# Optimization experiments

Measured on AMD Instinct MI355X. Metric: run time of the kernel, lower is better.

The kernel has to match this reference:

```python
import jax, jax.numpy as jnp
import numpy as np


def conv1d(x, w, b):
    # x: (N, Cin, W), w: (Cout, Cin, K) -> (N, Cout, W-K+1), VALID conv (torch Conv1d)
    y = jax.lax.conv_general_dilated(x, w, (1,), 'VALID', dimension_numbers=('NCH', 'OIH', 'NCH'))
    return y + b[None, :, None]


def cnn_block(x, w, b):
    # conv1d then MaxPool1d over the full valid length -> (N, Cout)
    return jnp.max(conv1d(x, w, b), axis=2)


def highway(x, Wp, bp, Wg, bg):
    p = jax.nn.relu(x @ Wp.T + bp)
    g = jax.nn.sigmoid(x @ Wg.T + bg)
    return g * p + (1.0 - g) * x


def lstm_masked(x, lens, Wih, Whh, bih, bhh):
    # x: (N, Wt, E); lens: (N,) valid lengths. Emulates pack_padded_sequence +
    # nn.LSTM + pad_packed_sequence: outputs are h_t for t < len, zeros after.
    N, Wt, _ = x.shape
    H = Whh.shape[1]
    bias = bih + bhh
    h0 = jnp.zeros((N, H), x.dtype)

    def step(carry, inp):
        xt, t = inp
        h, c = carry
        z = xt @ Wih.T + h @ Whh.T + bias  # (N, 4H), gate order i,f,g,o
        i, f, g, o = jnp.split(z, 4, axis=-1)
        c2 = jax.nn.sigmoid(f) * c + jax.nn.sigmoid(i) * jnp.tanh(g)
        h2 = jax.nn.sigmoid(o) * jnp.tanh(c2)
        valid = (t < lens)[:, None]
        h2 = jnp.where(valid, h2, h)
        c2 = jnp.where(valid, c2, c)
        return (h2, c2), jnp.where(valid, h2, jnp.zeros_like(h2))

    xs = jnp.moveaxis(x, 1, 0)  # (Wt, N, E)
    ts = jnp.arange(Wt)
    _, out = jax.lax.scan(step, (h0, h0), (xs, ts))
    return jnp.moveaxis(out, 0, 1)  # (N, Wt, H)


def setup_inputs() -> dict:
    key = jax.random.key(0)
    ks = jax.random.split(key, 32)
    B, T = 32, 48
    WL, WA, WE = 33, 50, 30
    EL, EA, EE, H = 300, 988, 20, 128
    CL, CA, CE = 128, 256, 64
    s = 0.02
    inp = {
        'x_lin': jax.random.normal(ks[0], (B, T, WL, EL), jnp.float32),
        'x_aco': jax.random.normal(ks[1], (B, T, WA, EA), jnp.float32),
        'x_emo': jax.random.normal(ks[2], (B, T, WE, EE), jnp.float32),
        'window_length': jax.random.randint(ks[3], (B, T), 0, WE).astype(jnp.int32) + 1,
        'length': jax.random.randint(ks[4], (B,), 1, T + 1).astype(jnp.int32),
        # CNN params
        'convL_w': s * jax.random.normal(ks[5], (CL, EL, 5), jnp.float32),
        'convL_b': jnp.zeros((CL,), jnp.float32),
        'convA_w': s * jax.random.normal(ks[6], (CA, EA, 10), jnp.float32),
        'convA_b': jnp.zeros((CA,), jnp.float32),
        'convE_w': s * jax.random.normal(ks[7], (CE, H, 3), jnp.float32),
        'convE_b': jnp.zeros((CE,), jnp.float32),
        # Highway params
        'hwL_Wp': s * jax.random.normal(ks[8], (CL, CL), jnp.float32),
        'hwL_bp': jnp.zeros((CL,), jnp.float32),
        'hwL_Wg': s * jax.random.normal(ks[9], (CL, CL), jnp.float32),
        'hwL_bg': jnp.zeros((CL,), jnp.float32),
        'hwA_Wp': s * jax.random.normal(ks[10], (CA, CA), jnp.float32),
        'hwA_bp': jnp.zeros((CA,), jnp.float32),
        'hwA_Wg': s * jax.random.normal(ks[11], (CA, CA), jnp.float32),
        'hwA_bg': jnp.zeros((CA,), jnp.float32),
        'hwE_Wp': s * jax.random.normal(ks[12], (CE, CE), jnp.float32),
        'hwE_bp': jnp.zeros((CE,), jnp.float32),
        'hwE_Wg': s * jax.random.normal(ks[13], (CE, CE), jnp.float32),
        'hwE_bg': jnp.zeros((CE,), jnp.float32),
        # LSTM params (nn.LSTM, 1 layer, batch_first)
        'lstm_Wih': s * jax.random.normal(ks[14], (4 * H, EE), jnp.float32),
        'lstm_Whh': s * jax.random.normal(ks[15], (4 * H, H), jnp.float32),
        'lstm_bih': jnp.zeros((4 * H,), jnp.float32),
        'lstm_bhh': jnp.zeros((4 * H,), jnp.float32),
    }
    return inp


def reference(x_lin, x_aco, x_emo, window_length, length,
              convL_w, convL_b, convA_w, convA_b, convE_w, convE_b,
              hwL_Wp, hwL_bp, hwL_Wg, hwL_bg,
              hwA_Wp, hwA_bp, hwA_Wg, hwA_bg,
              hwE_Wp, hwE_bp, hwE_Wg, hwE_bg,
              lstm_Wih, lstm_Whh, lstm_bih, lstm_bhh):
    B, T = x_lin.shape[:2]
    # Linguistic: per-window CNN + Highway (dropout = identity in eval)
    xl = x_lin.reshape(B * T, x_lin.shape[2], x_lin.shape[3]).transpose(0, 2, 1)  # (BT, 300, WL)
    outL = highway(cnn_block(xl, convL_w, convL_b), hwL_Wp, hwL_bp, hwL_Wg, hwL_bg)
    outL = outL.reshape(B, T, -1)
    # Acoustic
    xa = x_aco.reshape(B * T, x_aco.shape[2], x_aco.shape[3]).transpose(0, 2, 1)  # (BT, 988, WA)
    outA = highway(cnn_block(xa, convA_w, convA_b), hwA_Wp, hwA_bp, hwA_Wg, hwA_bg)
    outA = outA.reshape(B, T, -1)
    # Emotient: ragged per-window LSTM (packed semantics) -> CNN -> Highway
    xe = x_emo.reshape(B * T, x_emo.shape[2], x_emo.shape[3])  # (BT, WE, 20)
    lens = window_length.reshape(B * T)
    h = lstm_masked(xe, lens, lstm_Wih, lstm_Whh, lstm_bih, lstm_bhh)  # (BT, WE, 128)
    outE = highway(cnn_block(h.transpose(0, 2, 1), convE_w, convE_b), hwE_Wp, hwE_bp, hwE_Wg, hwE_bg)
    outE = outE.reshape(B, T, -1)
    # Concatenate modalities -> (B, T, 128+256+64) fed to the downstream head
    return jnp.concatenate([outL, outA, outE], axis=2)
```

## Files before the change

kernel.cpp:

```cpp
#include <hip/hip_runtime.h>
#include <hip/hip_bf16.h>
#include <math.h>

#define BTOT 1536
#define EL 300
#define ELP 320
#define WL_ 33
#define CL 128
#define LOUTL 29
#define KPL 1600
#define EA 988
#define EAP 992
#define WA_ 50
#define CA 256
#define LOUTA 41
#define KPA 9920
#define EE 20
#define WE_ 30
#define HH 128
#define CE 64
#define LOUTE 28
#define KPE 384
#define KDIML 1500
#define KDIMA 9880
#define KDIME 384

typedef __attribute__((ext_vector_type(4))) float f32x4;
typedef __attribute__((ext_vector_type(8))) short short8;

__device__ __forceinline__ unsigned short f2bf(float f) {
    unsigned int x = __float_as_uint(f);
    unsigned int r = (x + 0x7fffu + ((x >> 16) & 1u)) >> 16;
    return (unsigned short)r;
}

__device__ __forceinline__ float sigmf(float x) {
    return __builtin_amdgcn_rcpf(1.f + __expf(-x));
}
__device__ __forceinline__ float tanh_fast(float x) {
    return 1.f - 2.f * __builtin_amdgcn_rcpf(1.f + __expf(2.f * x));
}

#define GLD16(gp, lp) __builtin_amdgcn_global_load_lds( \
    (const __attribute__((address_space(1))) void*)(gp), \
    (__attribute__((address_space(3))) void*)(lp), 16, 0, 0)

template<int N> __device__ __forceinline__ void vmwait() {
    if constexpr (N == 0) asm volatile("s_waitcnt vmcnt(0)" ::: "memory");
    else if constexpr (N == 1) asm volatile("s_waitcnt vmcnt(1)" ::: "memory");
    else if constexpr (N == 2) asm volatile("s_waitcnt vmcnt(2)" ::: "memory");
    else if constexpr (N == 4) asm volatile("s_waitcnt vmcnt(4)" ::: "memory");
    else if constexpr (N == 5) asm volatile("s_waitcnt vmcnt(5)" ::: "memory");
    else if constexpr (N == 6) asm volatile("s_waitcnt vmcnt(6)" ::: "memory");
    else if constexpr (N == 8) asm volatile("s_waitcnt vmcnt(8)" ::: "memory");
    else static_assert(N == 0, "add case");
}

__device__ __forceinline__ void tr_one(const float* a, float* at, int R, int C, int idx) {
    int r = idx / C, c = idx - r * C;
    at[c * R + r] = a[idx];
}
template<int CIN, int CINP, int KW, int COUT, int KPAD>
__device__ __forceinline__ void wt_one(const float* w, unsigned short* wt, int idx) {
    int co = idx / KPAD;
    int p  = idx - co * KPAD;
    int k  = p / CINP;
    int c  = p - k * CINP;
    float v = 0.f;
    if (k < KW && c < CIN) v = w[(co * CIN + c) * KW + k];
    wt[idx] = f2bf(v);
}
template<bool BIG>
__global__ void prep_all(const float* hwL_Wp, float* WpTL, const float* hwL_Wg, float* WgTL,
                         const float* hwA_Wp, float* WpTA, const float* hwA_Wg, float* WgTA,
                         const float* hwE_Wp, float* WpTE, const float* hwE_Wg, float* WgTE,
                         const float* lstm_Wih, float* WihT, const float* lstm_Whh, float* WhhT,
                         const float* convL_w, unsigned short* wtL,
                         const float* convE_w, unsigned short* wtE,
                         const float* convA_w, unsigned short* wtA,
                         unsigned short* whh_bf, unsigned short* wihp_bf) {
    constexpr int S1 = 16384, S2 = 16384, S3 = 65536, S4 = 65536, S5 = 4096, S6 = 4096;
    constexpr int S7 = 512 * 20, S8 = 512 * 128;
    constexpr int S9 = 128 * KPL, S10 = 64 * KPE, S11 = 512 * 128, S12 = 512 * 32;
    constexpr int S13 = CA * KPA;
    constexpr int SMALL = S1 + S2 + S3 + S4 + S5 + S6 + S7 + S8;
    constexpr int TOTAL = BIG ? (SMALL + S9 + S10 + S11 + S12 + S13) : SMALL;
    int stride = gridDim.x * blockDim.x;
    for (int i = blockIdx.x * blockDim.x + threadIdx.x; i < TOTAL; i += stride) {
        int idx = i;
        if (idx < S1) { tr_one(hwL_Wp, WpTL, 128, 128, idx); continue; } idx -= S1;
        if (idx < S2) { tr_one(hwL_Wg, WgTL, 128, 128, idx); continue; } idx -= S2;
        if (idx < S3) { tr_one(hwA_Wp, WpTA, 256, 256, idx); continue; } idx -= S3;
        if (idx < S4) { tr_one(hwA_Wg, WgTA, 256, 256, idx); continue; } idx -= S4;
        if (idx < S5) { tr_one(hwE_Wp, WpTE, 64, 64, idx); continue; } idx -= S5;
        if (idx < S6) { tr_one(hwE_Wg, WgTE, 64, 64, idx); continue; } idx -= S6;
        if (idx < S7) { tr_one(lstm_Wih, WihT, 512, 20, idx); continue; } idx -= S7;
        if (idx < S8) { tr_one(lstm_Whh, WhhT, 512, 128, idx); continue; } idx -= S8;
        if constexpr (BIG) {
            if (idx < S9) { wt_one<EL, ELP, 5, CL, KPL>(convL_w, wtL, idx); continue; } idx -= S9;
            if (idx < S10) { wt_one<HH, HH, 3, CE, KPE>(convE_w, wtE, idx); continue; } idx -= S10;
            if (idx < S11) { whh_bf[idx] = f2bf(lstm_Whh[idx]); continue; } idx -= S11;
            if (idx < S12) { int col = idx >> 5, e = idx & 31;
                             wihp_bf[idx] = (e < 20) ? f2bf(lstm_Wih[col * 20 + e]) : (unsigned short)0;
                             continue; } idx -= S12;
            wt_one<EA, EAP, 10, CA, KPA>(convA_w, wtA, idx);
        }
    }
}

template<int CIN, int CINP>
__device__ __forceinline__ void cvt_chunk(const float* in, unsigned short* out, int idx) {
    constexpr int CH = CINP / 8;
    int row = idx / CH, c0 = (idx - row * CH) * 8;
    const float* src = in + (size_t)row * CIN + c0;
    union { short8 s; unsigned short u[8]; } o;
    if (c0 + 8 <= CIN) {
        float4 v0 = *(const float4*)src;
        float4 v1 = *(const float4*)(src + 4);
        o.u[0]=f2bf(v0.x); o.u[1]=f2bf(v0.y); o.u[2]=f2bf(v0.z); o.u[3]=f2bf(v0.w);
        o.u[4]=f2bf(v1.x); o.u[5]=f2bf(v1.y); o.u[6]=f2bf(v1.z); o.u[7]=f2bf(v1.w);
    } else {
        #pragma unroll
        for (int j = 0; j < 8; ++j) o.u[j] = (c0 + j < CIN) ? f2bf(src[j]) : (unsigned short)0;
    }
    *(short8*)(out + (size_t)row * CINP + c0) = o.s;
}

#define LSTM_BLOCKS 96
#define CVT_BLOCKS 1952

__global__ __launch_bounds__(512, 1)
void lstm_cvt(const float* __restrict__ x_emo,
              const unsigned short* __restrict__ wihp_bf, const unsigned short* __restrict__ whh_bf,
              const float* __restrict__ bih, const float* __restrict__ bhh,
              const int* __restrict__ lens, unsigned short* __restrict__ hbuf,
              const float* __restrict__ xa, const float* __restrict__ xl,
              unsigned short* __restrict__ outa, unsigned short* __restrict__ outl)
{
    __shared__ __align__(16) unsigned short xq[WE_ * 16 * 32];
    __shared__ __align__(16) char h_s[2 * 16 * HH * 2];

    if (blockIdx.x >= LSTM_BLOCKS) {
        constexpr int NAC = (BTOT * WA_) * (EAP / 8);
        constexpr int NLC = (BTOT * WL_) * (ELP / 8);
        int stride = CVT_BLOCKS * 512;
        for (int i = (blockIdx.x - LSTM_BLOCKS) * 512 + threadIdx.x; i < NAC + NLC; i += stride) {
            if (i < NAC) cvt_chunk<EA, EAP>(xa, outa, i);
            else         cvt_chunk<EL, ELP>(xl, outl, i - NAC);
        }
        return;
    }

    const int tid  = threadIdx.x;
    const int w    = tid >> 6;
    const int lane = tid & 63;
    const int lr   = lane & 15;
    const int lq   = lane >> 4;
    const int s0   = blockIdx.x * 16;
    const int c    = w * 16 + lr;

    short8 bfr[4][4];
    short8 bw[4];
    float bj[4];
    #pragma unroll
    for (int g = 0; g < 4; ++g) {
        int col = g * 128 + c;
        #pragma unroll
        for (int kt = 0; kt < 4; ++kt)
            bfr[g][kt] = *(const short8*)(whh_bf + (size_t)col * 128 + kt * 32 + lq * 8);
        bw[g] = *(const short8*)(wihp_bf + (size_t)col * 32 + lq * 8);
        bj[g] = bih[col] + bhh[col];
    }
    int len4[4];
    #pragma unroll
    for (int j = 0; j < 4; ++j) len4[j] = lens[s0 + lq * 4 + j];

    for (int i = tid; i < WE_ * 16 * 32; i += 512) {
        int t = i >> 9, r = (i >> 5) & 15, e = i & 31;
        xq[i] = (e < 20) ? f2bf(x_emo[(((size_t)(s0 + r) * WE_) + t) * 20 + e]) : (unsigned short)0;
    }
    for (int i = tid; i < 2048; i += 512) ((unsigned int*)h_s)[i] = 0u;

    float c_prev[4] = {0.f, 0.f, 0.f, 0.f};
    unsigned short hb_prev[4] = {0, 0, 0, 0};
    __syncthreads();

    for (int t = 0; t < WE_; ++t) {
        const char* hsr = h_s + (t & 1) * 4096;
        char* hsw = h_s + ((t & 1) ^ 1) * 4096;
        short8 ax = *(const short8*)((const char*)xq + (size_t)(t * 16 + lr) * 64 + lq * 16);
        short8 af[4];
        #pragma unroll
        for (int kt = 0; kt < 4; ++kt)
            af[kt] = *(const short8*)(hsr + ((lr * 256 + kt * 64 + lq * 16) ^ ((lr & 7) << 4)));
        f32x4 acc[4];
        #pragma unroll
        for (int g = 0; g < 4; ++g)
            acc[g] = __builtin_amdgcn_mfma_f32_16x16x32_bf16(ax, bw[g], (f32x4){0.f,0.f,0.f,0.f}, 0, 0, 0);
        #pragma unroll
        for (int kt = 0; kt < 4; ++kt)
            #pragma unroll
            for (int g = 0; g < 4; ++g)
                acc[g] = __builtin_amdgcn_mfma_f32_16x16x32_bf16(af[kt], bfr[g][kt], acc[g], 0, 0, 0);
        #pragma unroll
        for (int j = 0; j < 4; ++j) {
            int s = lq * 4 + j;
            float zi = acc[0][j] + bj[0];
            float zf = acc[1][j] + bj[1];
            float zg = acc[2][j] + bj[2];
            float zo = acc[3][j] + bj[3];
            float si = sigmf(zi), sf = sigmf(zf), so = sigmf(zo);
            float tg = tanh_fast(zg);
            float c2 = sf * c_prev[j] + si * tg;
            float h2 = so * tanh_fast(c2);
            bool valid = (t < len4[j]);
            c_prev[j] = valid ? c2 : c_prev[j];
            unsigned short h2b = f2bf(h2);
            unsigned short hn = valid ? h2b : hb_prev[j];
            hb_prev[j] = hn;
            *(unsigned short*)(hsw + (((s * HH + c) * 2) ^ ((s & 7) << 4))) = hn;
            hbuf[(((size_t)(s0 + s) * WE_) + t) * HH + c] = valid ? h2b : (unsigned short)0;
        }
        __syncthreads();
    }
}

template<int LOUT, int WIN, int CINP, int KW, int BN, int NS, int MFR, int COUT>
__global__ __launch_bounds__(256, 2)
void conv_pool_v10(const unsigned short* __restrict__ xb, const unsigned short* __restrict__ wt,
                   const float* __restrict__ bias, float* __restrict__ pooled)
{
    constexpr int CCH   = CINP / 32;
    constexpr int KB    = CINP * 2;
    constexpr int KTOTB = CINP * KW * 2;
    constexpr int NFR   = BN / 16;
    constexpr int B_IT  = BN / 64;
    constexpr int ABUF  = 4 * 64 * 64;
    constexpr int BBUF  = BN * 64;
    constexpr int CPQ   = (BTOT / 4) / 4;

    __shared__ __align__(16) char smem[2 * ABUF + 4 * BBUF];

    const int tid  = threadIdx.x;
    const int lane = tid & 63;
    const int wid  = tid >> 6;
    const int lr   = lane & 15;
    const int lq   = lane >> 4;
    const int lq16 = lq * 16;

    int m, n;
    if constexpr (NS == 2) {
        int xcd = blockIdx.x & 7;
        n = xcd & 1;
        m = (xcd >> 1) * CPQ + (blockIdx.x >> 3);
    } else {
        m = blockIdx.x; n = 0;
    }

    f32x4 acc[MFR][NFR];
    #pragma unroll
    for (int i = 0; i < MFR; ++i)
        #pragma unroll
        for (int j = 0; j < NFR; ++j) acc[i][j] = (f32x4){0.f, 0.f, 0.f, 0.f};

    const int aw_r = tid >> 2;
    const int aw   = (aw_r < WIN) ? aw_r : (WIN - 1);
    const int slot = tid & 3;
    const char* asrc[4];
    #pragma unroll
    for (int i = 0; i < 4; ++i)
        asrc[i] = (const char*)xb + ((size_t)((m * 4 + i) * WIN + aw)) * KB
                + ((slot * 16) ^ (((aw_r >> 1) & 3) << 4));
    const char* bsrc[B_IT];
    #pragma unroll
    for (int i = 0; i < B_IT; ++i) {
        int col = (tid + i * 256) >> 2;
        bsrc[i] = (const char*)wt + (size_t)(n * BN + col) * KTOTB
                + ((slot * 16) ^ (((col >> 1) & 3) << 4));
    }

    char* const abuf0 = smem;
    char* const abuf1 = smem + ABUF;
    char* const bbase = smem + 2 * ABUF;

    int cbo[NFR];
    #pragma unroll
    for (int nf = 0; nf < NFR; ++nf) {
        int cb = nf * 16 + lr;
        cbo[nf] = cb * 64 + (lq16 ^ (((cb >> 1) & 3) << 4));
    }

    #pragma unroll
    for (int i = 0; i < 4; ++i)
        GLD16(asrc[i], abuf0 + i * 4096 + tid * 16);
    #pragma unroll
    for (int s = 0; s < 3; ++s)
        #pragma unroll
        for (int i = 0; i < B_IT; ++i)
            GLD16(bsrc[i] + s * KB, bbase + s * BBUF + i * 4096 + tid * 16);
    vmwait<0>();
    __builtin_amdgcn_s_barrier();

    int bcur = 0;

#define STEP(KK, WN, TAIL) do {                                                    \
    const char* bb = bbase + bcur * BBUF;                                          \
    short8 afr[MFR];                                                               \
    _Pragma("unroll")                                                              \
    for (int o = 0; o < MFR; ++o) {                                                \
        int row = o * 16 + lr + (KK);                                              \
        afr[o] = *(const short8*)(awave + row * 64 + (lq16 ^ (((row >> 1) & 3) << 4))); \
    }                                                                              \
    short8 bf[NFR];                                                                \
    _Pragma("unroll")                                                              \
    for (int nf = 0; nf < NFR; ++nf) bf[nf] = *(const short8*)(bb + cbo[nf]);      \
    if (!(TAIL) || (KK) < KW - 3) {                                                \
        constexpr int k3_ = ((KK) + 3 < KW) ? (KK) + 3 : (KK) + 3 - KW;            \
        int boff = k3_ * KB + (((KK) + 3 < KW) ? ci : ci + 1) * 64;                \
        char* bstg = bbase + ((bcur + 3) & 3) * BBUF;                              \
        _Pragma("unroll")                                                          \
        for (int i = 0; i < B_IT; ++i)                                             \
            GLD16(bsrc[i] + boff, bstg + i * 4096 + tid * 16);                     \
    }                                                                              \
    if (!(TAIL)) {                                                                 \
        if (KW >= 8) {                                                             \
            if ((KK) < 4)                                                          \
                GLD16(asrc[(KK) & 3] + (size_t)(ci + 1) * 64, abn + ((KK) & 3) * 4096 + tid * 16); \
        } else if ((KK) == 0) {                                                    \
            _Pragma("unroll")                                                      \
            for (int i = 0; i < 4; ++i)                                            \
                GLD16(asrc[i] + (size_t)(ci + 1) * 64, abn + i * 4096 + tid * 16); \
        }                                                                          \
    }                                                                              \
    __builtin_amdgcn_s_setprio(1);                                                 \
    _Pragma("unroll")                                                              \
    for (int nf = 0; nf < NFR; ++nf)                                               \
        _Pragma("unroll")                                                          \
        for (int o = 0; o < MFR; ++o)                                              \
            acc[o][nf] = __builtin_amdgcn_mfma_f32_16x16x32_bf16(afr[o], bf[nf], acc[o][nf], 0, 0, 0); \
    __builtin_amdgcn_s_setprio(0);                                                 \
    vmwait<WN>();                                                                  \
    asm volatile("" ::: "memory");                                                 \
    __builtin_amdgcn_s_barrier();                                                  \
    bcur = (bcur + 1) & 3;                                                         \
} while (0)

    for (int ci = 0; ci < CCH - 1; ++ci) {
        const char* ab = (ci & 1) ? abuf1 : abuf0;
        char* abn = (ci & 1) ? abuf0 : abuf1;
        const char* awave = ab + wid * 4096;
        if constexpr (KW == 10) {
            STEP(0, 5, false); STEP(1, 6, false); STEP(2, 6, false); STEP(3, 6, false);
            STEP(4, 5, false); STEP(5, 4, false); STEP(6, 4, false); STEP(7, 4, false);
            STEP(8, 4, false); STEP(9, 4, false);
        } else if constexpr (KW == 5) {
            STEP(0, 8, false); STEP(1, 8, false); STEP(2, 4, false); STEP(3, 4, false); STEP(4, 4, false);
        } else {
            STEP(0, 6, false); STEP(1, 6, false); STEP(2, 2, false);
        }
    }
    {
        const int ci = CCH - 1;
        const char* ab = (ci & 1) ? abuf1 : abuf0;
        char* abn = (ci & 1) ? abuf0 : abuf1; (void)abn;
        const char* awave = ab + wid * 4096;
        if constexpr (KW == 10) {
            STEP(0, 4, true); STEP(1, 4, true); STEP(2, 4, true); STEP(3, 4, true);
            STEP(4, 4, true); STEP(5, 4, true); STEP(6, 4, true); STEP(7, 2, true);
            STEP(8, 0, true); STEP(9, 0, true);
        } else if constexpr (KW == 5) {
            STEP(0, 4, true); STEP(1, 4, true); STEP(2, 2, true); STEP(3, 0, true); STEP(4, 0, true);
        } else {
            STEP(0, 1, true); STEP(1, 0, true); STEP(2, 0, true);
        }
    }
#undef STEP

    const int bt = m * 4 + wid;
    #pragma unroll
    for (int nf = 0; nf < NFR; ++nf) {
        float mx = -INFINITY;
        #pragma unroll
        for (int o = 0; o < MFR; ++o) {
            int rb = o * 16 + lq * 4;
            #pragma unroll
            for (int j = 0; j < 4; ++j)
                if (rb + j < LOUT) mx = fmaxf(mx, acc[o][nf][j]);
        }
        mx = fmaxf(mx, __shfl_xor(mx, 16, 64));
        mx = fmaxf(mx, __shfl_xor(mx, 32, 64));
        if (lane < 16) {
            int col = n * BN + nf * 16 + lane;
            pooled[(size_t)bt * COUT + col] = mx + bias[col];
        }
    }
}

#define HWA_BLOCKS 192
#define HWL_BLOCKS 96
#define HWE_BLOCKS 48
__global__ __launch_bounds__(256)
void highway_v2(const float* __restrict__ pL, const float* __restrict__ pA, const float* __restrict__ pE,
                const float* __restrict__ WpTL, const float* __restrict__ bpL,
                const float* __restrict__ WgTL, const float* __restrict__ bgL,
                const float* __restrict__ WpTA, const float* __restrict__ bpA,
                const float* __restrict__ WgTA, const float* __restrict__ bgA,
                const float* __restrict__ WpTE, const float* __restrict__ bpE,
                const float* __restrict__ WgTE, const float* __restrict__ bgE,
                float* __restrict__ out) {
    __shared__ float xs[2048];
    int bx = blockIdx.x;
    int tid = threadIdx.x;
    if (bx < HWA_BLOCKS) {
        int bt0 = bx * 8;
        #pragma unroll
        for (int s = 0; s < 8; ++s) xs[s * 256 + tid] = pA[(size_t)(bt0 + s) * 256 + tid];
        __syncthreads();
        float p[8], g[8];
        #pragma unroll
        for (int s = 0; s < 8; ++s) { p[s] = bpA[tid]; g[s] = bgA[tid]; }
        for (int c = 0; c < 256; ++c) {
            float wp = WpTA[c * 256 + tid], wg = WgTA[c * 256 + tid];
            #pragma unroll
            for (int s = 0; s < 8; ++s) {
                float xv = xs[s * 256 + c];
                p[s] += xv * wp; g[s] += xv * wg;
            }
        }
        #pragma unroll
        for (int s = 0; s < 8; ++s) {
            float pp = fmaxf(p[s], 0.f);
            float gg = sigmf(g[s]);
            out[(size_t)(bt0 + s) * 448 + 128 + tid] = gg * pp + (1.f - gg) * xs[s * 256 + tid];
        }
    } else if (bx < HWA_BLOCKS + HWL_BLOCKS) {
        int bt0 = (bx - HWA_BLOCKS) * 16;
        for (int i = tid; i < 16 * 128; i += 256) xs[i] = pL[(size_t)bt0 * 128 + i];
        __syncthreads();
        int j = tid & 127, h = tid >> 7;
        float p[8], g[8];
        #pragma unroll
        for (int s = 0; s < 8; ++s) { p[s] = bpL[j]; g[s] = bgL[j]; }
        for (int c = 0; c < 128; ++c) {
            float wp = WpTL[c * 128 + j], wg = WgTL[c * 128 + j];
            #pragma unroll
            for (int s = 0; s < 8; ++s) {
                float xv = xs[(h * 8 + s) * 128 + c];
                p[s] += xv * wp; g[s] += xv * wg;
            }
        }
        #pragma unroll
        for (int s = 0; s < 8; ++s) {
            float pp = fmaxf(p[s], 0.f);
            float gg = sigmf(g[s]);
            out[(size_t)(bt0 + h * 8 + s) * 448 + j] = gg * pp + (1.f - gg) * xs[(h * 8 + s) * 128 + j];
        }
    } else {
        int bt0 = (bx - HWA_BLOCKS - HWL_BLOCKS) * 32;
        for (int i = tid; i < 32 * 64; i += 256) xs[i] = pE[(size_t)bt0 * 64 + i];
        __syncthreads();
        int j = tid & 63, grp = tid >> 6;
        float p[8], g[8];
        #pragma unroll
        for (int s = 0; s < 8; ++s) { p[s] = bpE[j]; g[s] = bgE[j]; }
        for (int c = 0; c < 64; ++c) {
            float wp = WpTE[c * 64 + j], wg = WgTE[c * 64 + j];
            #pragma unroll
            for (int s = 0; s < 8; ++s) {
                float xv = xs[(grp * 8 + s) * 64 + c];
                p[s] += xv * wp; g[s] += xv * wg;
            }
        }
        #pragma unroll
        for (int s = 0; s < 8; ++s) {
            float pp = fmaxf(p[s], 0.f);
            float gg = sigmf(g[s]);
            out[(size_t)(bt0 + grp * 8 + s) * 448 + 384 + j] = gg * pp + (1.f - gg) * xs[(grp * 8 + s) * 64 + j];
        }
    }
}

__global__ __launch_bounds__(512)
void lstm_kernel_f32(const float* __restrict__ x, const int* __restrict__ lens,
                     const float* __restrict__ WihT, const float* __restrict__ WhhT,
                     const float* __restrict__ bih, const float* __restrict__ bhh,
                     float* __restrict__ hout) {
    int bt = blockIdx.x;
    int j  = threadIdx.x;
    __shared__ float xs[WE_][EE];
    __shared__ __align__(16) float hs[HH];
    __shared__ float zs[512];
    for (int idx = j; idx < WE_ * EE; idx += 512)
        ((float*)xs)[idx] = x[(size_t)bt * WE_ * EE + idx];
    if (j < HH) hs[j] = 0.f;
    float wih[EE];
    #pragma unroll
    for (int e = 0; e < EE; ++e) wih[e] = WihT[e * 512 + j];
    float whh[HH];
    #pragma unroll
    for (int h = 0; h < HH; ++h) whh[h] = WhhT[h * 512 + j];
    float bjv = bih[j] + bhh[j];
    float c_reg = 0.f;
    int len = lens[bt];
    __syncthreads();
    for (int t = 0; t < WE_; ++t) {
        float z = bjv;
        #pragma unroll
        for (int e = 0; e < EE; ++e) z += wih[e] * xs[t][e];
        const float4* h4 = (const float4*)hs;
        #pragma unroll
        for (int q = 0; q < HH / 4; ++q) {
            float4 hv = h4[q];
            z += whh[4*q+0] * hv.x + whh[4*q+1] * hv.y
               + whh[4*q+2] * hv.z + whh[4*q+3] * hv.w;
        }
        zs[j] = z;
        __syncthreads();
        if (j < HH) {
            float zi = zs[j], zf = zs[HH + j], zg = zs[2*HH + j], zo = zs[3*HH + j];
            float si = 1.f / (1.f + expf(-zi));
            float sf = 1.f / (1.f + expf(-zf));
            float so = 1.f / (1.f + expf(-zo));
            float tg = tanhf(zg);
            float c2 = sf * c_reg + si * tg;
            float h2 = so * tanhf(c2);
            bool valid = (t < len);
            float hn = valid ? h2 : hs[j];
            c_reg    = valid ? c2 : c_reg;
            hout[((size_t)bt * WE_ + t) * HH + j] = valid ? h2 : 0.f;
            hs[j] = hn;
        }
        __syncthreads();
    }
}

template<int CIN, int WIN, int COUT, int KDIM, int LOUT>
__global__ __launch_bounds__(256)
void conv_pool_simple(const float* __restrict__ x, const float* __restrict__ w,
                      const float* __restrict__ bias, float* __restrict__ pooled)
{
    constexpr int KW = KDIM / CIN;
    int bt = blockIdx.x;
    int co = blockIdx.y * 64 + (threadIdx.x & 63);
    int seg = threadIdx.x >> 6;
    __shared__ float part[4][64];
    float m = -INFINITY;
    for (int l = seg; l < LOUT; l += 4) {
        float acc = 0.f;
        for (int k = 0; k < KW; ++k) {
            const float* xr = x + ((size_t)bt * WIN + l + k) * CIN;
            const float* wr = w + ((size_t)co * CIN) * KW + k;
            for (int cc = 0; cc < CIN; ++cc) acc += xr[cc] * wr[(size_t)cc * KW];
        }
        m = fmaxf(m, acc);
    }
    part[seg][threadIdx.x & 63] = m;
    __syncthreads();
    if (threadIdx.x < 64) {
        float mm = fmaxf(fmaxf(part[0][threadIdx.x], part[1][threadIdx.x]),
                         fmaxf(part[2][threadIdx.x], part[3][threadIdx.x]));
        pooled[(size_t)bt * COUT + co] = mm + bias[co];
    }
}

static inline int cdiv(int a, int b) { return (a + b - 1) / b; }

extern "C" void kernel_launch(void* const* d_in, const int* in_sizes, int n_in,
                              void* d_out, int out_size, void* d_ws, size_t ws_size,
                              hipStream_t stream) {
    const float* x_lin  = (const float*)d_in[0];
    const float* x_aco  = (const float*)d_in[1];
    const float* x_emo  = (const float*)d_in[2];
    const int*   wlen   = (const int*)  d_in[3];
    const float* convL_w = (const float*)d_in[5];
    const float* convL_b = (const float*)d_in[6];
    const float* convA_w = (const float*)d_in[7];
    const float* convA_b = (const float*)d_in[8];
    const float* convE_w = (const float*)d_in[9];
    const float* convE_b = (const float*)d_in[10];
    const float* hwL_Wp = (const float*)d_in[11];
    const float* hwL_bp = (const float*)d_in[12];
    const float* hwL_Wg = (const float*)d_in[13];
    const float* hwL_bg = (const float*)d_in[14];
    const float* hwA_Wp = (const float*)d_in[15];
    const float* hwA_bp = (const float*)d_in[16];
    const float* hwA_Wg = (const float*)d_in[17];
    const float* hwA_bg = (const float*)d_in[18];
    const float* hwE_Wp = (const float*)d_in[19];
    const float* hwE_bp = (const float*)d_in[20];
    const float* hwE_Wg = (const float*)d_in[21];
    const float* hwE_bg = (const float*)d_in[22];
    const float* lstm_Wih = (const float*)d_in[23];
    const float* lstm_Whh = (const float*)d_in[24];
    const float* lstm_bih = (const float*)d_in[25];
    const float* lstm_bhh = (const float*)d_in[26];
    float* out = (float*)d_out;

    char* p0 = (char*)d_ws;
    char* p = p0;
    auto alloc = [&](size_t bytes) { char* r = p; p += (bytes + 255) & ~(size_t)255; return r; };
    float* WpTL = (float*)alloc((size_t)CL * CL * 4);
    float* WgTL = (float*)alloc((size_t)CL * CL * 4);
    float* WpTA = (float*)alloc((size_t)CA * CA * 4);
    float* WgTA = (float*)alloc((size_t)CA * CA * 4);
    float* WpTE = (float*)alloc((size_t)CE * CE * 4);
    float* WgTE = (float*)alloc((size_t)CE * CE * 4);
    float* WihT = (float*)alloc((size_t)EE * 512 * 4);
    float* WhhT = (float*)alloc((size_t)HH * 512 * 4);
    unsigned short* whh_bf  = (unsigned short*)alloc((size_t)512 * 128 * 2);
    unsigned short* wihp_bf = (unsigned short*)alloc((size_t)512 * 32 * 2);
    void*  hbuf = (void*)alloc((size_t)BTOT * WE_ * HH * 4);
    float* pL   = (float*)alloc((size_t)BTOT * CL * 4);
    float* pA   = (float*)alloc((size_t)BTOT * CA * 4);
    float* pE   = (float*)alloc((size_t)BTOT * CE * 4);
    unsigned short* wtA = (unsigned short*)alloc((size_t)CA * KPA * 2);
    unsigned short* wtL = (unsigned short*)alloc((size_t)CL * KPL * 2);
    unsigned short* wtE = (unsigned short*)alloc((size_t)CE * KPE * 2);
    unsigned short* xlin_p = (unsigned short*)alloc((size_t)BTOT * WL_ * ELP * 2 + 64);
    unsigned short* xaco_p = (unsigned short*)alloc((size_t)BTOT * WA_ * EAP * 2 + 64);
    size_t need = (size_t)(p - p0);
    bool big = ws_size >= need;

    if (big) {
        prep_all<true><<<2048, 256, 0, stream>>>(hwL_Wp, WpTL, hwL_Wg, WgTL, hwA_Wp, WpTA, hwA_Wg, WgTA,
                                                 hwE_Wp, WpTE, hwE_Wg, WgTE, lstm_Wih, WihT, lstm_Whh, WhhT,
                                                 convL_w, wtL, convE_w, wtE, convA_w, wtA, whh_bf, wihp_bf);
        lstm_cvt<<<LSTM_BLOCKS + CVT_BLOCKS, 512, 0, stream>>>(
            x_emo, wihp_bf, whh_bf, lstm_bih, lstm_bhh, wlen, (unsigned short*)hbuf,
            x_aco, x_lin, xaco_p, xlin_p);
        conv_pool_v10<LOUTA, WA_, EAP, 10, 128, 2, 3, CA>
            <<<768, 256, 0, stream>>>(xaco_p, wtA, convA_b, pA);
        conv_pool_v10<LOUTL, WL_, ELP, 5, 128, 1, 2, CL>
            <<<384, 256, 0, stream>>>(xlin_p, wtL, convL_b, pL);
        conv_pool_v10<LOUTE, WE_, HH, 3, 64, 1, 2, CE>
            <<<384, 256, 0, stream>>>((const unsigned short*)hbuf, wtE, convE_b, pE);
        highway_v2<<<HWA_BLOCKS + HWL_BLOCKS + HWE_BLOCKS, 256, 0, stream>>>(
            pL, pA, pE, WpTL, hwL_bp, WgTL, hwL_bg, WpTA, hwA_bp, WgTA, hwA_bg,
            WpTE, hwE_bp, WgTE, hwE_bg, out);
    } else {
        prep_all<false><<<2048, 256, 0, stream>>>(hwL_Wp, WpTL, hwL_Wg, WgTL, hwA_Wp, WpTA, hwA_Wg, WgTA,
                                                  hwE_Wp, WpTE, hwE_Wg, WgTE, lstm_Wih, WihT, lstm_Whh, WhhT,
                                                  convL_w, wtL, convE_w, wtE, convA_w, wtA, whh_bf, wihp_bf);
        lstm_kernel_f32<<<BTOT, 512, 0, stream>>>(x_emo, wlen, WihT, WhhT, lstm_bih, lstm_bhh, (float*)hbuf);
        conv_pool_simple<EA, WA_, CA, KDIMA, LOUTA>
            <<<dim3(BTOT, CA / 64), 256, 0, stream>>>(x_aco, convA_w, convA_b, pA);
        conv_pool_simple<EL, WL_, CL, KDIML, LOUTL>
            <<<dim3(BTOT, CL / 64), 256, 0, stream>>>(x_lin, convL_w, convL_b, pL);
        conv_pool_simple<HH, WE_, CE, KDIME, LOUTE>
            <<<dim3(BTOT, CE / 64), 256, 0, stream>>>((const float*)hbuf, convE_w, convE_b, pE);
        highway_v2<<<HWA_BLOCKS + HWL_BLOCKS + HWE_BLOCKS, 256, 0, stream>>>(
            pL, pA, pE, WpTL, hwL_bp, WgTL, hwL_bg, WpTA, hwA_bp, WgTA, hwA_bg,
            WpTE, hwE_bp, WgTE, hwE_bg, out);
    }
}
```

Before: 559.7 us.

## Overlap linguistic bf16 conversion with acoustic conv and deepen B-weight pipeline

The linguistic input's fp32-to-bf16 conversion moves out of the LSTM/convert kernel and into extra blocks of a new dedicated acoustic conv kernel, so it runs alongside the acoustic convolution. The new acoustic kernel uses a 5-slot B-weight ring with 3-ahead prefetch and a barrier only every other K step, which should cut synchronization and load stalls. This adds shared memory per block, which may lower occupancy, and the converter blocks compete with the conv blocks for bandwidth.

```diff
diff --git a/kernel.cpp b/kernel.cpp
--- a/kernel.cpp
+++ b/kernel.cpp
@@ -49,6 +49,7 @@
     if constexpr (N == 0) asm volatile("s_waitcnt vmcnt(0)" ::: "memory");
     else if constexpr (N == 1) asm volatile("s_waitcnt vmcnt(1)" ::: "memory");
     else if constexpr (N == 2) asm volatile("s_waitcnt vmcnt(2)" ::: "memory");
+    else if constexpr (N == 3) asm volatile("s_waitcnt vmcnt(3)" ::: "memory");
     else if constexpr (N == 4) asm volatile("s_waitcnt vmcnt(4)" ::: "memory");
     else if constexpr (N == 5) asm volatile("s_waitcnt vmcnt(5)" ::: "memory");
     else if constexpr (N == 6) asm volatile("s_waitcnt vmcnt(6)" ::: "memory");
@@ -127,27 +128,23 @@
 }
 
 #define LSTM_BLOCKS 96
-#define CVT_BLOCKS 1952
+#define CVTA_BLOCKS 1440
 
 __global__ __launch_bounds__(512, 1)
 void lstm_cvt(const float* __restrict__ x_emo,
               const unsigned short* __restrict__ wihp_bf, const unsigned short* __restrict__ whh_bf,
               const float* __restrict__ bih, const float* __restrict__ bhh,
               const int* __restrict__ lens, unsigned short* __restrict__ hbuf,
-              const float* __restrict__ xa, const float* __restrict__ xl,
-              unsigned short* __restrict__ outa, unsigned short* __restrict__ outl)
+              const float* __restrict__ xa, unsigned short* __restrict__ outa)
 {
     __shared__ __align__(16) unsigned short xq[WE_ * 16 * 32];
     __shared__ __align__(16) char h_s[2 * 16 * HH * 2];
 
     if (blockIdx.x >= LSTM_BLOCKS) {
         constexpr int NAC = (BTOT * WA_) * (EAP / 8);
-        constexpr int NLC = (BTOT * WL_) * (ELP / 8);
-        int stride = CVT_BLOCKS * 512;
-        for (int i = (blockIdx.x - LSTM_BLOCKS) * 512 + threadIdx.x; i < NAC + NLC; i += stride) {
-            if (i < NAC) cvt_chunk<EA, EAP>(xa, outa, i);
-            else         cvt_chunk<EL, ELP>(xl, outl, i - NAC);
-        }
+        int stride = CVTA_BLOCKS * 512;
+        for (int i = (blockIdx.x - LSTM_BLOCKS) * 512 + threadIdx.x; i < NAC; i += stride)
+            cvt_chunk<EA, EAP>(xa, outa, i);
         return;
     }
 
@@ -222,6 +219,174 @@
             hbuf[(((size_t)(s0 + s) * WE_) + t) * HH + c] = valid ? h2b : (unsigned short)0;
         }
         __syncthreads();
+    }
+}
+
+#define CONVA_BLOCKS 768
+#define CVTL_BLOCKS 512
+__global__ __launch_bounds__(256, 2)
+void conv_a_v11(const unsigned short* __restrict__ xb, const unsigned short* __restrict__ wt,
+                const float* __restrict__ bias, float* __restrict__ pooled,
+                const float* __restrict__ xl, unsigned short* __restrict__ outl)
+{
+    constexpr int LOUT = LOUTA, WIN = WA_, CINP = EAP, BN = 128, COUT = CA;
+    constexpr int CCH  = CINP / 32;
+    constexpr int KB   = CINP * 2;
+    constexpr int KTOTB = CINP * 10 * 2;
+    constexpr int ABUF = 4 * 64 * 64;
+    constexpr int BBUF = BN * 64;
+    constexpr int CPQ  = 96;
+
+    __shared__ __align__(16) char smem[2 * ABUF + 5 * BBUF];
+
+    if (blockIdx.x >= CONVA_BLOCKS) {
+        constexpr int NLC = (BTOT * WL_) * (ELP / 8);
+        int stride = CVTL_BLOCKS * 256;
+        for (int i = (blockIdx.x - CONVA_BLOCKS) * 256 + threadIdx.x; i < NLC; i += stride)
+            cvt_chunk<EL, ELP>(xl, outl, i);
+        return;
+    }
+
+    const int tid  = threadIdx.x;
+    const int lane = tid & 63;
+    const int wid  = tid >> 6;
+    const int lr   = lane & 15;
+    const int lq   = lane >> 4;
+    const int lq16 = lq * 16;
+
+    int xcd = blockIdx.x & 7;
+    int n = xcd & 1;
+    int m = (xcd >> 1) * CPQ + (blockIdx.x >> 3);
+
+    f32x4 acc[3][8];
+    #pragma unroll
+    for (int i = 0; i < 3; ++i)
+        #pragma unroll
+        for (int j = 0; j < 8; ++j) acc[i][j] = (f32x4){0.f, 0.f, 0.f, 0.f};
+
+    const int aw_r = tid >> 2;
+    const int aw   = (aw_r < WIN) ? aw_r : (WIN - 1);
+    const int slot = tid & 3;
+    const char* asrc[4];
+    #pragma unroll
+    for (int i = 0; i < 4; ++i)
+        asrc[i] = (const char*)xb + ((size_t)((m * 4 + i) * WIN + aw)) * KB
+                + ((slot * 16) ^ (((aw_r >> 1) & 3) << 4));
+    const char* bsrc[2];
+    #pragma unroll
+    for (int i = 0; i < 2; ++i) {
+        int col = (tid + i * 256) >> 2;
+        bsrc[i] = (const char*)wt + (size_t)(n * BN + col) * KTOTB
+                + ((slot * 16) ^ (((col >> 1) & 3) << 4));
+    }
+
+    char* const abuf0 = smem;
+    char* const abuf1 = smem + ABUF;
+    char* const bbase = smem + 2 * ABUF;
+
+    int cbo[8];
+    #pragma unroll
+    for (int nf = 0; nf < 8; ++nf) {
+        int cb = nf * 16 + lr;
+        cbo[nf] = cb * 64 + (lq16 ^ (((cb >> 1) & 3) << 4));
+    }
+
+    #pragma unroll
+    for (int i = 0; i < 4; ++i)
+        GLD16(asrc[i], abuf0 + i * 4096 + tid * 16);
+    #pragma unroll
+    for (int s = 0; s < 3; ++s) {
+        GLD16(bsrc[0] + s * KB, bbase + s * BBUF + tid * 16);
+        GLD16(bsrc[1] + s * KB, bbase + s * BBUF + 4096 + tid * 16);
+    }
+    vmwait<0>();
+    __builtin_amdgcn_s_barrier();
+
+    int bcur = 0;
+
+#define VSTEP(KK, DOA, DOBAR, WN, DOBSTG, CHN) do {                                \
+    const char* bb = bbase + bcur * BBUF;                                          \
+    short8 afr[3];                                                                 \
+    _Pragma("unroll")                                                              \
+    for (int o = 0; o < 3; ++o) {                                                  \
+        int row = o * 16 + lr + (KK);                                              \
+        afr[o] = *(const short8*)(awave + row * 64 + (lq16 ^ (((row >> 1) & 3) << 4))); \
+    }                                                                              \
+    short8 bf[8];                                                                  \
+    _Pragma("unroll")                                                              \
+    for (int nf = 0; nf < 8; ++nf) bf[nf] = *(const short8*)(bb + cbo[nf]);        \
+    if (DOBSTG) {                                                                  \
+        constexpr int K3 = ((KK) + 3 < 10) ? (KK) + 3 : (KK) - 7;                  \
+        int boff = K3 * KB + (CHN) * 64;                                           \
+        int b3 = bcur + 3; if (b3 >= 5) b3 -= 5;                                   \
+        char* bstg = bbase + b3 * BBUF;                                            \
+        GLD16(bsrc[0] + boff, bstg + tid * 16);                                    \
+        GLD16(bsrc[1] + boff, bstg + 4096 + tid * 16);                             \
+    }                                                                              \
+    if (DOA) GLD16(asrc[(KK) - 5] + (size_t)(ci + 1) * 64,                         \
+                   abn + ((KK) - 5) * 4096 + tid * 16);                            \
+    __builtin_amdgcn_s_setprio(1);                                                 \
+    _Pragma("unroll")                                                              \
+    for (int nf = 0; nf < 8; ++nf)                                                 \
+        _Pragma("unroll")                                                          \
+        for (int o = 0; o < 3; ++o)                                                \
+            acc[o][nf] = __builtin_amdgcn_mfma_f32_16x16x32_bf16(afr[o], bf[nf], acc[o][nf], 0, 0, 0); \
+    __builtin_amdgcn_s_setprio(0);                                                 \
+    if (DOBAR) { vmwait<WN>(); asm volatile("" ::: "memory");                      \
+                 __builtin_amdgcn_s_barrier(); }                                   \
+    bcur = (bcur == 4) ? 0 : bcur + 1;                                             \
+} while (0)
+
+    for (int ci = 0; ci < CCH - 1; ++ci) {
+        const char* ab = (ci & 1) ? abuf1 : abuf0;
+        char* abn = (ci & 1) ? abuf0 : abuf1;
+        const char* awave = ab + wid * 4096;
+        VSTEP(0, false, false, 0, true, ci);
+        VSTEP(1, false, true,  2, true, ci);
+        VSTEP(2, false, false, 0, true, ci);
+        VSTEP(3, false, true,  2, true, ci);
+        VSTEP(4, false, false, 0, true, ci);
+        VSTEP(5, true,  true,  3, true, ci);
+        VSTEP(6, true,  false, 0, true, ci);
+        VSTEP(7, true,  true,  3, true, ci + 1);
+        VSTEP(8, true,  false, 0, true, ci + 1);
+        VSTEP(9, false, true,  2, true, ci + 1);
+    }
+    {
+        const int ci = CCH - 1;
+        const char* ab = (ci & 1) ? abuf1 : abuf0;
+        char* abn = (ci & 1) ? abuf0 : abuf1; (void)abn;
+        const char* awave = ab + wid * 4096;
+        VSTEP(0, false, false, 0, true,  ci);
+        VSTEP(1, false, true,  2, true,  ci);
+        VSTEP(2, false, false, 0, true,  ci);
+        VSTEP(3, false, true,  2, true,  ci);
+        VSTEP(4, false, false, 0, true,  ci);
+        VSTEP(5, false, true,  2, true,  ci);
+        VSTEP(6, false, false, 0, true,  ci);
+        VSTEP(7, false, true,  0, false, ci);
+        VSTEP(8, false, false, 0, false, ci);
+        VSTEP(9, false, true,  0, false, ci);
+    }
+#undef VSTEP
+
+    const int bt = m * 4 + wid;
+    #pragma unroll
+    for (int nf = 0; nf < 8; ++nf) {
+        float mx = -INFINITY;
+        #pragma unroll
+        for (int o = 0; o < 3; ++o) {
+            int rb = o * 16 + lq * 4;
+            #pragma unroll
+            for (int j = 0; j < 4; ++j)
+                if (rb + j < LOUT) mx = fmaxf(mx, acc[o][nf][j]);
+        }
+        mx = fmaxf(mx, __shfl_xor(mx, 16, 64));
+        mx = fmaxf(mx, __shfl_xor(mx, 32, 64));
+        if (lane < 16) {
+            int col = n * BN + nf * 16 + lane;
+            pooled[(size_t)bt * COUT + col] = mx + bias[col];
+        }
     }
 }
 
@@ -349,11 +514,7 @@
         const char* ab = (ci & 1) ? abuf1 : abuf0;
         char* abn = (ci & 1) ? abuf0 : abuf1;
         const char* awave = ab + wid * 4096;
-        if constexpr (KW == 10) {
-            STEP(0, 5, false); STEP(1, 6, false); STEP(2, 6, false); STEP(3, 6, false);
-            STEP(4, 5, false); STEP(5, 4, false); STEP(6, 4, false); STEP(7, 4, false);
-            STEP(8, 4, false); STEP(9, 4, false);
-        } else if constexpr (KW == 5) {
+        if constexpr (KW == 5) {
             STEP(0, 8, false); STEP(1, 8, false); STEP(2, 4, false); STEP(3, 4, false); STEP(4, 4, false);
         } else {
             STEP(0, 6, false); STEP(1, 6, false); STEP(2, 2, false);
@@ -364,11 +525,7 @@
         const char* ab = (ci & 1) ? abuf1 : abuf0;
         char* abn = (ci & 1) ? abuf0 : abuf1; (void)abn;
         const char* awave = ab + wid * 4096;
-        if constexpr (KW == 10) {
-            STEP(0, 4, true); STEP(1, 4, true); STEP(2, 4, true); STEP(3, 4, true);
-            STEP(4, 4, true); STEP(5, 4, true); STEP(6, 4, true); STEP(7, 2, true);
-            STEP(8, 0, true); STEP(9, 0, true);
-        } else if constexpr (KW == 5) {
+        if constexpr (KW == 5) {
             STEP(0, 4, true); STEP(1, 4, true); STEP(2, 2, true); STEP(3, 0, true); STEP(4, 0, true);
         } else {
             STEP(0, 1, true); STEP(1, 0, true); STEP(2, 0, true);
@@ -625,11 +782,11 @@
         prep_all<true><<<2048, 256, 0, stream>>>(hwL_Wp, WpTL, hwL_Wg, WgTL, hwA_Wp, WpTA, hwA_Wg, WgTA,
                                                  hwE_Wp, WpTE, hwE_Wg, WgTE, lstm_Wih, WihT, lstm_Whh, WhhT,
                                                  convL_w, wtL, convE_w, wtE, convA_w, wtA, whh_bf, wihp_bf);
-        lstm_cvt<<<LSTM_BLOCKS + CVT_BLOCKS, 512, 0, stream>>>(
+        lstm_cvt<<<LSTM_BLOCKS + CVTA_BLOCKS, 512, 0, stream>>>(
             x_emo, wihp_bf, whh_bf, lstm_bih, lstm_bhh, wlen, (unsigned short*)hbuf,
-            x_aco, x_lin, xaco_p, xlin_p);
-        conv_pool_v10<LOUTA, WA_, EAP, 10, 128, 2, 3, CA>
-            <<<768, 256, 0, stream>>>(xaco_p, wtA, convA_b, pA);
+            x_aco, xaco_p);
+        conv_a_v11<<<CONVA_BLOCKS + CVTL_BLOCKS, 256, 0, stream>>>(
+            xaco_p, wtA, convA_b, pA, x_lin, xlin_p);
         conv_pool_v10<LOUTL, WL_, ELP, 5, 128, 1, 2, CL>
             <<<384, 256, 0, stream>>>(xlin_p, wtL, convL_b, pL);
         conv_pool_v10<LOUTE, WE_, HH, 3, 64, 1, 2, CE>
```

Measured after the change: 518.6 us. -7.3%, faster.
